# Kernel tuning notes

Measured on AMD Instinct MI355X. Metric: run time of the kernel, lower is better.

The kernel has to match this reference:

```python
import jax, jax.numpy as jnp
import numpy as np

MASK_VALUE = 0.0  # default `mask=0` scalar in the original forward


def setup_inputs() -> dict:
    key = jax.random.key(0)
    kq, kk, kv = jax.random.split(key, 3)
    b, n, d_k, d_v = 8, 2048, 64, 64
    q = jax.random.normal(kq, (b, n, d_k), dtype=jnp.float32)
    k = jax.random.normal(kk, (b, n, d_k), dtype=jnp.float32)
    v = jax.random.normal(kv, (b, n, d_v), dtype=jnp.float32)
    return {"q": q, "k": k, "v": v}


def reference(q, k, v):
    d_k = q.shape[-1]
    temper = jnp.asarray(d_k, q.dtype) ** 0.5
    # scores: (b, n, n)
    attn = jnp.einsum('bqd,bkd->bqk', q, k) / temper
    # equality-based masking: positions whose score exactly equals the
    # scalar `mask` (default 0) are set to -inf before softmax.
    attn = jnp.where(attn == MASK_VALUE, -jnp.inf, attn)
    # NOTE: the original code calls `attn.masked_fill(look_ahead_mask==0, -inf)`
    # WITHOUT assignment, so the look-ahead mask is a no-op; we omit it faithfully.
    attn = jax.nn.softmax(attn, axis=-1)
    out = jnp.einsum('bqk,bkd->bqd', attn, v)  # (b, n, d_v)
    return out
```

## Files before the change

### kernel.cpp

```cpp
#include <hip/hip_runtime.h>
#include <hip/hip_bf16.h>

typedef __bf16 bf16_t;
typedef bf16_t bf16x2 __attribute__((ext_vector_type(2)));
typedef bf16_t bf16x4 __attribute__((ext_vector_type(4)));
typedef bf16_t bf16x8 __attribute__((ext_vector_type(8)));
typedef float  floatx4  __attribute__((ext_vector_type(4)));
typedef float  floatx16 __attribute__((ext_vector_type(16)));

constexpr int B = 8, N = 2048, D = 64;
constexpr int TSTR = 65;

__global__ __launch_bounds__(256)
void prepass_kernel(const float* __restrict__ k, const float* __restrict__ v,
                    bf16_t* __restrict__ kb, bf16_t* __restrict__ vt) {
    __shared__ float t[64 * TSTR];
    const int tid = threadIdx.x;
    const int b   = blockIdx.x & 7;
    const int r0  = ((blockIdx.x >> 3) & 31) * 64;
    if ((blockIdx.x >> 8) == 0) {
        const float* src = k + ((size_t)b * N + r0) * D;
        bf16_t* dst = kb + ((size_t)b * N + r0) * D;
        #pragma unroll
        for (int p = 0; p < 4; ++p) {
            int e = (tid + p * 256) * 4;
            floatx4 f = *(const floatx4*)(src + e);
            bf16x4 o;
            #pragma unroll
            for (int j = 0; j < 4; ++j) o[j] = (bf16_t)f[j];
            *(bf16x4*)(dst + e) = o;
        }
    } else {
        const float* vb = v + ((size_t)b * N + r0) * D;
        #pragma unroll
        for (int p = 0; p < 4; ++p) {
            int e = (tid + p * 256) * 4;
            int row = e >> 6, col = e & 63;
            floatx4 f = *(const floatx4*)(vb + e);
            #pragma unroll
            for (int j = 0; j < 4; ++j) t[(col + j) * TSTR + row] = f[j];
        }
        __syncthreads();
        bf16_t* ob = vt + (size_t)b * D * N + r0;
        #pragma unroll
        for (int p = 0; p < 4; ++p) {
            int e = (tid + p * 256) * 4;
            int drow = e >> 6, kcol = e & 63;
            bf16x4 o;
            #pragma unroll
            for (int j = 0; j < 4; ++j) o[j] = (bf16_t)t[drow * TSTR + kcol + j];
            *(bf16x4*)(ob + (size_t)drow * N + kcol) = o;
        }
    }
}

__global__ __launch_bounds__(1024, 4)
void attn_kernel(const float* __restrict__ q, const bf16_t* __restrict__ kb,
                 const bf16_t* __restrict__ vt, float* __restrict__ out) {
    __shared__ char smem[131072];

    const int tid  = threadIdx.x;
    const int lane = tid & 63;
    const int wave = tid >> 6;
    const int qg   = wave >> 3;
    const int cg   = wave & 7;
    const int h    = lane >> 5;
    const int l31  = lane & 31;
    const int sw   = l31 & 7;

    const int b  = blockIdx.x & 7;
    const int q0 = (blockIdx.x >> 3) * 64 + qg * 32;

    const bf16_t* kbb = kb + (size_t)b * N * D;
    const bf16_t* vbb = vt + (size_t)b * D * N;

    bf16x8 qf[4];
    {
        const float* qp = q + ((size_t)b * N + q0 + l31) * D + h * 8;
        #pragma unroll
        for (int kd = 0; kd < 4; ++kd) {
            floatx4 f0 = *(const floatx4*)(qp + kd * 16);
            floatx4 f1 = *(const floatx4*)(qp + kd * 16 + 4);
            bf16x8 t;
            #pragma unroll
            for (int j = 0; j < 4; ++j) { t[j] = (bf16_t)f0[j]; t[j + 4] = (bf16_t)f1[j]; }
            qf[kd] = t;
        }
    }

    floatx16 o_acc[2];
    #pragma unroll
    for (int d = 0; d < 2; ++d)
        #pragma unroll
        for (int i = 0; i < 16; ++i) o_acc[d][i] = 0.f;
    float l_run = 0.f;

    bf16x8 kreg[2], vreg[2];
    #pragma unroll
    for (int p = 0; p < 2; ++p) {
        int e = (tid + p * 1024) * 8;
        kreg[p] = *(const bf16x8*)(kbb + e);
        vreg[p] = *(const bf16x8*)(vbb + (size_t)(e >> 8) * N + (e & 255));
    }

    #pragma unroll 1
    for (int it = 0; it < N / 256; ++it) {
        char* base = smem + (it & 1) * 65536;
        bf16_t* lds_k = (bf16_t*)base;
        bf16_t* lds_v = (bf16_t*)(base + 32768);

        #pragma unroll
        for (int p = 0; p < 2; ++p) {
            int e  = (tid + p * 1024) * 8;
            int kr = e >> 6, kg = (e >> 3) & 7;
            *(bf16x8*)&lds_k[kr * 64 + ((kg ^ (kr & 7)) << 3)] = kreg[p];
            int vr = e >> 8, vg = (e >> 3) & 31;
            *(bf16x8*)&lds_v[vr * 256 + ((vg ^ (vr & 7)) << 3)] = vreg[p];
        }
        __syncthreads();

        if (it + 1 < N / 256) {
            const int kv1 = (it + 1) * 256;
            #pragma unroll
            for (int p = 0; p < 2; ++p) {
                int e = (tid + p * 1024) * 8;
                kreg[p] = *(const bf16x8*)(kbb + (size_t)kv1 * D + e);
                vreg[p] = *(const bf16x8*)(vbb + (size_t)(e >> 8) * N + kv1 + (e & 255));
            }
        }

        floatx16 s;
        #pragma unroll
        for (int i = 0; i < 16; ++i) s[i] = 0.f;
        #pragma unroll
        for (int kd = 0; kd < 4; ++kd) {
            bf16x8 kf = *(const bf16x8*)&lds_k[(cg * 32 + l31) * 64 + (((2 * kd + h) ^ sw) << 3)];
            s = __builtin_amdgcn_mfma_f32_32x32x16_bf16(kf, qf[kd], s, 0, 0, 0);
        }

        int q8[8];
        #pragma unroll
        for (int g = 0; g < 8; ++g) {
            union { int i; bf16x2 h2; } u;
            #pragma unroll
            for (int j = 0; j < 2; ++j) {
                float x = s[2 * g + j] * 0.125f;
                float p = (x == 0.0f) ? 0.0f : __expf(x);
                l_run += p;
                u.h2[j] = (bf16_t)p;
            }
            q8[g] = u.i;
        }

        #pragma unroll
        for (int s2 = 0; s2 < 2; ++s2) {
            int r0 = __shfl_xor(q8[4 * s2 + 0], 32);
            int r1 = __shfl_xor(q8[4 * s2 + 1], 32);
            int r2 = __shfl_xor(q8[4 * s2 + 2], 32);
            int r3 = __shfl_xor(q8[4 * s2 + 3], 32);
            union { int i4[4]; bf16x8 v; } bf;
            bf.i4[0] = h ? r2 : q8[4 * s2 + 0];
            bf.i4[1] = h ? r3 : q8[4 * s2 + 1];
            bf.i4[2] = h ? q8[4 * s2 + 2] : r0;
            bf.i4[3] = h ? q8[4 * s2 + 3] : r1;
            #pragma unroll
            for (int dblk = 0; dblk < 2; ++dblk) {
                bf16x8 va = *(const bf16x8*)&lds_v[(dblk * 32 + l31) * 256 +
                                                   (((cg * 4 + s2 * 2 + h) ^ sw) << 3)];
                o_acc[dblk] = __builtin_amdgcn_mfma_f32_32x32x16_bf16(va, bf.v, o_acc[dblk], 0, 0, 0);
            }
        }
    }

    __syncthreads();

    l_run += __shfl_xor(l_run, 32);

    if (cg > 0) {
        float* ob = (float*)smem + (size_t)qg * 14336 + (size_t)(cg - 1) * 2048;
        #pragma unroll
        for (int dblk = 0; dblk < 2; ++dblk)
            #pragma unroll
            for (int i = 0; i < 16; ++i) {
                const int d = (i & 3) + 8 * (i >> 2) + 4 * h + dblk * 32;
                ob[d * 32 + l31] = o_acc[dblk][i];
            }
        if (h == 0) ((float*)(smem + 114688))[qg * 224 + (cg - 1) * 32 + l31] = l_run;
    }
    __syncthreads();
    if (cg == 0) {
        const float* lb = (const float*)(smem + 114688) + qg * 224;
        float lsum = l_run;
        #pragma unroll
        for (int gg = 0; gg < 7; ++gg) lsum += lb[gg * 32 + l31];
        const float inv_l = 1.0f / lsum;
        const float* ob = (const float*)smem + (size_t)qg * 14336;
        float* op = out + ((size_t)b * N + q0 + l31) * D;
        #pragma unroll
        for (int dblk = 0; dblk < 2; ++dblk)
            #pragma unroll
            for (int g = 0; g < 4; ++g) {
                const int d0 = 8 * g + 4 * h + dblk * 32;
                floatx4 o4;
                #pragma unroll
                for (int j = 0; j < 4; ++j) {
                    float sum = o_acc[dblk][4 * g + j];
                    #pragma unroll
                    for (int gg = 0; gg < 7; ++gg)
                        sum += ob[gg * 2048 + (d0 + j) * 32 + l31];
                    o4[j] = sum * inv_l;
                }
                *(floatx4*)(op + d0) = o4;
            }
    }
}

extern "C" void kernel_launch(void* const* d_in, const int* in_sizes, int n_in,
                              void* d_out, int out_size, void* d_ws, size_t ws_size,
                              hipStream_t stream) {
    const float* q = (const float*)d_in[0];
    const float* k = (const float*)d_in[1];
    const float* v = (const float*)d_in[2];
    float* out = (float*)d_out;
    bf16_t* kb = (bf16_t*)d_ws;
    bf16_t* vt = (bf16_t*)((char*)d_ws + (size_t)B * N * D * 2);

    hipLaunchKernelGGL(prepass_kernel, dim3(512), dim3(256), 0, stream, k, v, kb, vt);
    hipLaunchKernelGGL(attn_kernel, dim3(256), dim3(1024), 0, stream, q, kb, vt, out);
}
```

Before: 86.39 us.

## Split KV range across blocks with separate merge kernel for partial outputs

Restructures the attention kernel from 256 blocks of 16 waves, each splitting 256-key chunks across 8 column groups, into 512 blocks of 8 waves. Each block handles 128 queries over one quarter of the keys, using 64-key tiles and a much smaller LDS footprint. Unnormalized partial outputs and row sums go to workspace, and a new merge kernel adds the four splits and normalizes. This aims to raise occupancy and cut the heavy in-block 8-way LDS reduction. In exchange it adds an extra kernel launch and global traffic for the partial outputs.

```diff
diff --git a/kernel.cpp b/kernel.cpp
--- a/kernel.cpp
+++ b/kernel.cpp
@@ -54,22 +54,26 @@
     }
 }
 
-__global__ __launch_bounds__(1024, 4)
+__global__ __launch_bounds__(512, 4)
 void attn_kernel(const float* __restrict__ q, const bf16_t* __restrict__ kb,
-                 const bf16_t* __restrict__ vt, float* __restrict__ out) {
-    __shared__ char smem[131072];
+                 const bf16_t* __restrict__ vt, float* __restrict__ osp,
+                 float* __restrict__ lsp) {
+    __shared__ char smem[33280];
 
     const int tid  = threadIdx.x;
     const int lane = tid & 63;
     const int wave = tid >> 6;
-    const int qg   = wave >> 3;
-    const int cg   = wave & 7;
+    const int qg   = wave >> 1;
+    const int cg   = wave & 1;
     const int h    = lane >> 5;
     const int l31  = lane & 31;
     const int sw   = l31 & 7;
 
-    const int b  = blockIdx.x & 7;
-    const int q0 = (blockIdx.x >> 3) * 64 + qg * 32;
+    const int b     = blockIdx.x & 7;
+    const int qblk  = (blockIdx.x >> 3) & 15;
+    const int split = blockIdx.x >> 7;
+    const int q0 = qblk * 128 + qg * 32;
+    const int kv_base = split * 512;
 
     const bf16_t* kbb = kb + (size_t)b * N * D;
     const bf16_t* vbb = vt + (size_t)b * D * N;
@@ -95,38 +99,27 @@
         for (int i = 0; i < 16; ++i) o_acc[d][i] = 0.f;
     float l_run = 0.f;
 
-    bf16x8 kreg[2], vreg[2];
-    #pragma unroll
-    for (int p = 0; p < 2; ++p) {
-        int e = (tid + p * 1024) * 8;
-        kreg[p] = *(const bf16x8*)(kbb + e);
-        vreg[p] = *(const bf16x8*)(vbb + (size_t)(e >> 8) * N + (e & 255));
-    }
+    const int e = tid * 8;
+    bf16x8 kreg = *(const bf16x8*)(kbb + (size_t)kv_base * D + e);
+    bf16x8 vreg = *(const bf16x8*)(vbb + (size_t)(e >> 6) * N + kv_base + (e & 63));
+
+    const int er = e >> 6, eg = (e >> 3) & 7;
+    const int esw = ((eg ^ (er & 7)) << 3);
 
     #pragma unroll 1
-    for (int it = 0; it < N / 256; ++it) {
-        char* base = smem + (it & 1) * 65536;
+    for (int it = 0; it < 8; ++it) {
+        char* base = smem + (it & 1) * 16384;
         bf16_t* lds_k = (bf16_t*)base;
-        bf16_t* lds_v = (bf16_t*)(base + 32768);
-
-        #pragma unroll
-        for (int p = 0; p < 2; ++p) {
-            int e  = (tid + p * 1024) * 8;
-            int kr = e >> 6, kg = (e >> 3) & 7;
-            *(bf16x8*)&lds_k[kr * 64 + ((kg ^ (kr & 7)) << 3)] = kreg[p];
-            int vr = e >> 8, vg = (e >> 3) & 31;
-            *(bf16x8*)&lds_v[vr * 256 + ((vg ^ (vr & 7)) << 3)] = vreg[p];
-        }
+        bf16_t* lds_v = (bf16_t*)(base + 8192);
+
+        *(bf16x8*)&lds_k[er * 64 + esw] = kreg;
+        *(bf16x8*)&lds_v[er * 64 + esw] = vreg;
         __syncthreads();
 
-        if (it + 1 < N / 256) {
-            const int kv1 = (it + 1) * 256;
-            #pragma unroll
-            for (int p = 0; p < 2; ++p) {
-                int e = (tid + p * 1024) * 8;
-                kreg[p] = *(const bf16x8*)(kbb + (size_t)kv1 * D + e);
-                vreg[p] = *(const bf16x8*)(vbb + (size_t)(e >> 8) * N + kv1 + (e & 255));
-            }
+        if (it + 1 < 8) {
+            const int kv1 = kv_base + (it + 1) * 64;
+            kreg = *(const bf16x8*)(kbb + (size_t)kv1 * D + e);
+            vreg = *(const bf16x8*)(vbb + (size_t)(e >> 6) * N + kv1 + (e & 63));
         }
 
         floatx16 s;
@@ -165,7 +158,7 @@
             bf.i4[3] = h ? q8[4 * s2 + 3] : r1;
             #pragma unroll
             for (int dblk = 0; dblk < 2; ++dblk) {
-                bf16x8 va = *(const bf16x8*)&lds_v[(dblk * 32 + l31) * 256 +
+                bf16x8 va = *(const bf16x8*)&lds_v[(dblk * 32 + l31) * 64 +
                                                    (((cg * 4 + s2 * 2 + h) ^ sw) << 3)];
                 o_acc[dblk] = __builtin_amdgcn_mfma_f32_32x32x16_bf16(va, bf.v, o_acc[dblk], 0, 0, 0);
             }
@@ -176,8 +169,11 @@
 
     l_run += __shfl_xor(l_run, 32);
 
-    if (cg > 0) {
-        float* ob = (float*)smem + (size_t)qg * 14336 + (size_t)(cg - 1) * 2048;
+    float* o_buf = (float*)smem;
+    float* l_buf = (float*)(smem + 32768);
+
+    if (cg == 1) {
+        float* ob = o_buf + qg * 2048;
         #pragma unroll
         for (int dblk = 0; dblk < 2; ++dblk)
             #pragma unroll
@@ -185,17 +181,14 @@
                 const int d = (i & 3) + 8 * (i >> 2) + 4 * h + dblk * 32;
                 ob[d * 32 + l31] = o_acc[dblk][i];
             }
-        if (h == 0) ((float*)(smem + 114688))[qg * 224 + (cg - 1) * 32 + l31] = l_run;
+        if (h == 0) l_buf[qg * 32 + l31] = l_run;
     }
     __syncthreads();
     if (cg == 0) {
-        const float* lb = (const float*)(smem + 114688) + qg * 224;
-        float lsum = l_run;
-        #pragma unroll
-        for (int gg = 0; gg < 7; ++gg) lsum += lb[gg * 32 + l31];
-        const float inv_l = 1.0f / lsum;
-        const float* ob = (const float*)smem + (size_t)qg * 14336;
-        float* op = out + ((size_t)b * N + q0 + l31) * D;
+        const float lsum = l_run + l_buf[qg * 32 + l31];
+        const float* ob = o_buf + qg * 2048;
+        const size_t pb = (size_t)(split * 8 + b) * 16 + qblk;
+        float* op = osp + (pb * 128 + qg * 32 + l31) * 64;
         #pragma unroll
         for (int dblk = 0; dblk < 2; ++dblk)
             #pragma unroll
@@ -203,16 +196,31 @@
                 const int d0 = 8 * g + 4 * h + dblk * 32;
                 floatx4 o4;
                 #pragma unroll
-                for (int j = 0; j < 4; ++j) {
-                    float sum = o_acc[dblk][4 * g + j];
-                    #pragma unroll
-                    for (int gg = 0; gg < 7; ++gg)
-                        sum += ob[gg * 2048 + (d0 + j) * 32 + l31];
-                    o4[j] = sum * inv_l;
-                }
+                for (int j = 0; j < 4; ++j)
+                    o4[j] = o_acc[dblk][4 * g + j] + ob[(d0 + j) * 32 + l31];
                 *(floatx4*)(op + d0) = o4;
             }
-    }
+        if (h == 0) lsp[pb * 128 + qg * 32 + l31] = lsum;
+    }
+}
+
+__global__ __launch_bounds__(256)
+void merge_kernel(const float* __restrict__ osp, const float* __restrict__ lsp,
+                  float* __restrict__ out) {
+    const int idx = blockIdx.x * 256 + threadIdx.x;
+    const int b   = idx >> 17;
+    const int rem = idx & 131071;
+    const int qblk = rem >> 13;
+    const int ql   = (rem >> 6) & 127;
+    const int d    = rem & 63;
+    float o = 0.f, l = 0.f;
+    #pragma unroll
+    for (int s = 0; s < 4; ++s) {
+        const size_t pb = (size_t)(s * 8 + b) * 16 + qblk;
+        o += osp[(pb * 128 + ql) * 64 + d];
+        l += lsp[pb * 128 + ql];
+    }
+    out[idx] = o / l;
 }
 
 extern "C" void kernel_launch(void* const* d_in, const int* in_sizes, int n_in,
@@ -224,7 +232,10 @@
     float* out = (float*)d_out;
     bf16_t* kb = (bf16_t*)d_ws;
     bf16_t* vt = (bf16_t*)((char*)d_ws + (size_t)B * N * D * 2);
+    float*  osp = (float*)((char*)d_ws + (4u << 20));
+    float*  lsp = (float*)((char*)d_ws + (24u << 20));
 
     hipLaunchKernelGGL(prepass_kernel, dim3(512), dim3(256), 0, stream, k, v, kb, vt);
-    hipLaunchKernelGGL(attn_kernel, dim3(256), dim3(1024), 0, stream, q, kb, vt, out);
-}
+    hipLaunchKernelGGL(attn_kernel, dim3(512), dim3(512), 0, stream, q, kb, vt, osp, lsp);
+    hipLaunchKernelGGL(merge_kernel, dim3((B * N * D) / 256), dim3(256), 0, stream, osp, lsp, out);
+}
```

Result: slower. 93.24 us (+7.9%).
